# Optimization experiments

Hardware: AMD Instinct MI355X
Metric: run time of the kernel (lower is better)

Reference implementation:

```python
import jax, jax.numpy as jnp
import numpy as np

H = 4      # heads
C = 32     # out channels per head (hidden_channels)
G = 64     # num graphs


def transformer_conv(x, src, dst, Wq, bq, Wk, bk, Wv, bv, Ws, bs):
    # PyG TransformerConv, concat=False, root_weight=True, beta=False.
    N = x.shape[0]
    q = (x @ Wq + bq).reshape(N, H, C)
    k = (x @ Wk + bk).reshape(N, H, C)
    v = (x @ Wv + bv).reshape(N, H, C)
    qe = q[dst]            # [E,H,C] gather target queries
    ke = k[src]            # [E,H,C] gather source keys
    ve = v[src]            # [E,H,C] gather source values
    alpha = (qe * ke).sum(-1) / jnp.sqrt(jnp.asarray(C, x.dtype))  # [E,H]
    amax = jax.ops.segment_max(alpha, dst, num_segments=N)          # [N,H]
    a = jnp.exp(alpha - amax[dst])
    denom = jax.ops.segment_sum(a, dst, num_segments=N)             # [N,H]
    a = a / (denom[dst] + 1e-16)
    out = jax.ops.segment_sum(ve * a[..., None], dst, num_segments=N)  # [N,H,C]
    out = out.mean(axis=1)          # concat=False -> head average
    return out + x @ Ws + bs        # root skip


def setup_inputs() -> dict:
    key = jax.random.key(0)
    ks = jax.random.split(key, 24)
    N, E, Fin = 40000, 640000, 128
    x = jax.random.normal(ks[0], (N, Fin), dtype=jnp.float32)
    edge_index = jax.random.randint(ks[1], (2, E), 0, N, dtype=jnp.int64)
    batch = jnp.sort(jax.random.randint(ks[2], (N,), 0, G, dtype=jnp.int64))
    s = 0.05
    w = lambda k, shp: jax.random.normal(k, shp, dtype=jnp.float32) * s
    d = {"x": x, "edge_index": edge_index, "batch": batch,
         "Wq1": w(ks[3], (Fin, H * C)), "bq1": w(ks[4], (H * C,)),
         "Wk1": w(ks[5], (Fin, H * C)), "bk1": w(ks[6], (H * C,)),
         "Wv1": w(ks[7], (Fin, H * C)), "bv1": w(ks[8], (H * C,)),
         "Ws1": w(ks[9], (Fin, C)), "bs1": w(ks[10], (C,)),
         "Wq2": w(ks[11], (C, H * C)), "bq2": w(ks[12], (H * C,)),
         "Wk2": w(ks[13], (C, H * C)), "bk2": w(ks[14], (H * C,)),
         "Wv2": w(ks[15], (C, H * C)), "bv2": w(ks[16], (H * C,)),
         "Ws2": w(ks[17], (C, C)), "bs2": w(ks[18], (C,)),
         "Wlin": w(ks[19], (C, 16)), "blin": w(ks[20], (16,))}
    return d


def reference(x, edge_index, batch,
              Wq1, bq1, Wk1, bk1, Wv1, bv1, Ws1, bs1,
              Wq2, bq2, Wk2, bk2, Wv2, bv2, Ws2, bs2,
              Wlin, blin):
    src, dst = edge_index[0], edge_index[1]
    h = transformer_conv(x, src, dst, Wq1, bq1, Wk1, bk1, Wv1, bv1, Ws1, bs1)
    h = jax.nn.relu(h)
    h = transformer_conv(h, src, dst, Wq2, bq2, Wk2, bk2, Wv2, bv2, Ws2, bs2)
    # global mean pool over graphs
    sums = jax.ops.segment_sum(h, batch, num_segments=G)                  # [G,C]
    cnts = jax.ops.segment_sum(jnp.ones((h.shape[0],), h.dtype), batch, num_segments=G)
    pooled = sums / jnp.maximum(cnts, 1.0)[:, None]
    return pooled @ Wlin + blin
```

## Files before the change

kernel.cpp:

```cpp
#include <hip/hip_runtime.h>
#include <hip/hip_bf16.h>
#include <hip/hip_fp16.h>
#include <math.h>

#define HH 4
#define CC 32
#define HC 128
#define GG 64

typedef _Float16 f16x2 __attribute__((ext_vector_type(2)));
typedef _Float16 f16x8 __attribute__((ext_vector_type(8)));
typedef float f32x4 __attribute__((ext_vector_type(4)));

__device__ __forceinline__ f16x2 u2h(unsigned u) {
    union { unsigned u; f16x2 h; } x; x.u = u; return x.h;
}
__device__ __forceinline__ unsigned pkh(float a, float b) {
    __half2 h = __floats2half2_rn(a, b);
    union { __half2 h; unsigned u; } x; x.h = h; return x.u;
}
__device__ __forceinline__ f16x8 uq2h8(uint4 u) {
    union { uint4 u; f16x8 h; } x; x.u = u; return x.h;
}

__global__ void cvt_f2h_kernel(const float* __restrict__ in, unsigned* __restrict__ out, int n4)
{
    int i = blockIdx.x * 256 + threadIdx.x;
    if (i < n4) {
        float4 f = ((const float4*)in)[i];
        ((uint2*)out)[i] = make_uint2(pkh(f.x, f.y), pkh(f.z, f.w));
    }
}

__device__ __forceinline__ void wfrag_item(const float* __restrict__ Wq, const float* __restrict__ Wk,
    const float* __restrict__ Wv, const float* __restrict__ Ws,
    uint4* __restrict__ wfrag, int KS, int idx)
{
    int lane = idx & 63;
    int t = idx >> 6;
    int ks = t % KS, ct = t / KS;
    int r = lane & 15, g = lane >> 4;
    const float* W; int c, stride;
    if (ct < 8)       { W = Wq; c = ct * 16 + r;        stride = HC; }
    else if (ct < 16) { W = Wk; c = (ct - 8) * 16 + r;  stride = HC; }
    else if (ct < 24) { W = Wv; c = (ct - 16) * 16 + r; stride = HC; }
    else              { W = Ws; c = (ct - 24) * 16 + r; stride = CC; }
    unsigned u[4];
    #pragma unroll
    for (int jj = 0; jj < 4; ++jj) {
        int k = ks * 32 + g * 8 + jj * 2;
        u[jj] = pkh(W[(size_t)k * stride + c], W[(size_t)(k + 1) * stride + c]);
    }
    wfrag[idx] = make_uint4(u[0], u[1], u[2], u[3]);
}

__global__ void wfrag_both_kernel(
    const float* __restrict__ Wq1, const float* __restrict__ Wk1,
    const float* __restrict__ Wv1, const float* __restrict__ Ws1, uint4* __restrict__ wfrag1,
    const float* __restrict__ Wq2, const float* __restrict__ Wk2,
    const float* __restrict__ Wv2, const float* __restrict__ Ws2, uint4* __restrict__ wfrag2)
{
    int idx = blockIdx.x * 256 + threadIdx.x;
    const int N1 = 26 * 4 * 64;
    const int N2 = 26 * 1 * 64;
    if (idx < N1) wfrag_item(Wq1, Wk1, Wv1, Ws1, wfrag1, 4, idx);
    else if (idx < N1 + N2) wfrag_item(Wq2, Wk2, Wv2, Ws2, wfrag2, 1, idx - N1);
}

template<int KDIM>
__global__ __launch_bounds__(256) void qkv_mfma_kernel(
    const ushort* __restrict__ xh, const uint4* __restrict__ wfrag,
    const float* __restrict__ bq, const float* __restrict__ bk,
    const float* __restrict__ bv, const float* __restrict__ bs,
    unsigned* __restrict__ qh, uint4* __restrict__ kv4, float* __restrict__ skip,
    int N)
{
    constexpr int KS = KDIM / 32;
    const int lane = threadIdx.x & 63;
    const int wv = threadIdx.x >> 6;
    const int n0 = (blockIdx.x * 4 + wv) * 16;
    if (n0 >= N) return;
    const int r = lane & 15, g = lane >> 4;
    const int node = n0 + r;

    f16x8 a[KS];
    #pragma unroll
    for (int ks = 0; ks < KS; ++ks)
        a[ks] = uq2h8(*(const uint4*)&xh[(size_t)node * KDIM + ks * 32 + g * 8]);

    if (blockIdx.y == 0) {
        const float SC2 = 0.25500526806584186f;
        f32x4 acc[10];
        #pragma unroll
        for (int i = 0; i < 10; ++i) acc[i] = (f32x4){0.f, 0.f, 0.f, 0.f};
        #pragma unroll
        for (int i = 0; i < 8; ++i)
            #pragma unroll
            for (int ks = 0; ks < KS; ++ks) {
                f16x8 w = uq2h8(wfrag[((size_t)i * KS + ks) * 64 + lane]);
                acc[i] = __builtin_amdgcn_mfma_f32_16x16x32_f16(w, a[ks], acc[i], 0, 0, 0);
            }
        #pragma unroll
        for (int i = 0; i < 2; ++i)
            #pragma unroll
            for (int ks = 0; ks < KS; ++ks) {
                f16x8 w = uq2h8(wfrag[((size_t)(24 + i) * KS + ks) * 64 + lane]);
                acc[8 + i] = __builtin_amdgcn_mfma_f32_16x16x32_f16(w, a[ks], acc[8 + i], 0, 0, 0);
            }
        if (node < N) {
            #pragma unroll
            for (int i = 0; i < 8; ++i) {
                float4 bb = *(const float4*)&bq[i * 16 + g * 4];
                uint2 o = make_uint2(pkh((acc[i][0] + bb.x) * SC2, (acc[i][1] + bb.y) * SC2),
                                     pkh((acc[i][2] + bb.z) * SC2, (acc[i][3] + bb.w) * SC2));
                *(uint2*)&qh[(size_t)node * 64 + i * 8 + g * 2] = o;
            }
            #pragma unroll
            for (int i = 0; i < 2; ++i) {
                float4 bb = *(const float4*)&bs[i * 16 + g * 4];
                float4 o = make_float4(acc[8 + i][0] + bb.x, acc[8 + i][1] + bb.y,
                                       acc[8 + i][2] + bb.z, acc[8 + i][3] + bb.w);
                *(float4*)&skip[(size_t)node * CC + i * 16 + g * 4] = o;
            }
        }
    } else {
        f32x4 acck[8], accv[8];
        #pragma unroll
        for (int i = 0; i < 8; ++i) { acck[i] = (f32x4){0.f,0.f,0.f,0.f}; accv[i] = (f32x4){0.f,0.f,0.f,0.f}; }
        #pragma unroll
        for (int i = 0; i < 8; ++i)
            #pragma unroll
            for (int ks = 0; ks < KS; ++ks) {
                f16x8 wk = uq2h8(wfrag[((size_t)(8 + i) * KS + ks) * 64 + lane]);
                acck[i] = __builtin_amdgcn_mfma_f32_16x16x32_f16(wk, a[ks], acck[i], 0, 0, 0);
                f16x8 wvf = uq2h8(wfrag[((size_t)(16 + i) * KS + ks) * 64 + lane]);
                accv[i] = __builtin_amdgcn_mfma_f32_16x16x32_f16(wvf, a[ks], accv[i], 0, 0, 0);
            }
        if (node < N) {
            #pragma unroll
            for (int i = 0; i < 8; ++i) {
                float4 bbk = *(const float4*)&bk[i * 16 + g * 4];
                float4 bbv = *(const float4*)&bv[i * 16 + g * 4];
                uint4 o;
                o.x = pkh(acck[i][0] + bbk.x, acck[i][1] + bbk.y);
                o.y = pkh(acck[i][2] + bbk.z, acck[i][3] + bbk.w);
                o.z = pkh(accv[i][0] + bbv.x, accv[i][1] + bbv.y);
                o.w = pkh(accv[i][2] + bbv.z, accv[i][3] + bbv.w);
                kv4[(size_t)node * 32 + i * 4 + g] = o;
            }
        }
    }
}

__global__ void deg_kernel(const int* __restrict__ dst, int* __restrict__ deg, int E)
{
    int e = blockIdx.x * blockDim.x + threadIdx.x;
    if (e < E) atomicAdd(&deg[dst[e]], 1);
}

__global__ void bsum_kernel(const int* __restrict__ deg, int* __restrict__ bsum, int N)
{
    int base = blockIdx.x * 1024;
    int tid = threadIdx.x;
    int s = 0;
    for (int i = base + tid; i < base + 1024 && i < N; i += 256) s += deg[i];
    #pragma unroll
    for (int ofs = 32; ofs > 0; ofs >>= 1) s += __shfl_xor(s, ofs, 64);
    __shared__ int ws[4];
    int wid = tid >> 6;
    if ((tid & 63) == 0) ws[wid] = s;
    __syncthreads();
    if (tid == 0) bsum[blockIdx.x] = ws[0] + ws[1] + ws[2] + ws[3];
}

__global__ void bscan_kernel(int* __restrict__ bsum, int* __restrict__ off, int nb, int N)
{
    int i = threadIdx.x;
    int val = (i < nb) ? bsum[i] : 0;
    int v = val;
    #pragma unroll
    for (int ofs = 1; ofs < 64; ofs <<= 1) {
        int t = __shfl_up(v, ofs, 64);
        if (i >= ofs) v += t;
    }
    if (i < nb) bsum[i] = v - val;
    if (i == 63) off[N] = v;
}

__global__ void scan2_kernel(const int* __restrict__ deg, const int* __restrict__ bsum,
                             int* __restrict__ off, int* __restrict__ cursor, int N)
{
    int base = blockIdx.x * 1024;
    int tid = threadIdx.x;
    int idx = base + tid * 4;
    int d0 = (idx     < N) ? deg[idx]     : 0;
    int d1 = (idx + 1 < N) ? deg[idx + 1] : 0;
    int d2 = (idx + 2 < N) ? deg[idx + 2] : 0;
    int d3 = (idx + 3 < N) ? deg[idx + 3] : 0;
    int tsum = d0 + d1 + d2 + d3;
    int v = tsum;
    int lane = tid & 63;
    #pragma unroll
    for (int ofs = 1; ofs < 64; ofs <<= 1) {
        int t = __shfl_up(v, ofs, 64);
        if (lane >= ofs) v += t;
    }
    __shared__ int wsum[4];
    int wid = tid >> 6;
    if (lane == 63) wsum[wid] = v;
    __syncthreads();
    int wbase = 0;
    for (int w = 0; w < wid; ++w) wbase += wsum[w];
    int excl = bsum[blockIdx.x] + wbase + (v - tsum);
    if (idx     < N) { off[idx]     = excl;                cursor[idx]     = excl; }
    if (idx + 1 < N) { off[idx + 1] = excl + d0;           cursor[idx + 1] = excl + d0; }
    if (idx + 2 < N) { off[idx + 2] = excl + d0 + d1;      cursor[idx + 2] = excl + d0 + d1; }
    if (idx + 3 < N) { off[idx + 3] = excl + d0 + d1 + d2; cursor[idx + 3] = excl + d0 + d1 + d2; }
}

__global__ void fill_kernel(const int* __restrict__ src, const int* __restrict__ dst,
                            int* __restrict__ cursor, int* __restrict__ esrc, int E)
{
    int e = blockIdx.x * blockDim.x + threadIdx.x;
    if (e < E) {
        int d = dst[e];
        int pos = atomicAdd(&cursor[d], 1);
        esrc[pos] = src[e];
    }
}

template<int MODE>
__global__ __launch_bounds__(128) void attn_kernel(const unsigned* __restrict__ qh,
    const uint4* __restrict__ kv4, const int* __restrict__ off, const int* __restrict__ esrc,
    const float* __restrict__ skip, void* __restrict__ hout, int N)
{
    const int wave = threadIdx.x >> 6;
    const int lane = threadIdx.x & 63;
    const int n = blockIdx.x * 2 + wave;
    if (n >= N) return;
    const int half = lane >> 5;
    const int j = lane & 31;

    uint2 qv = *(const uint2*)&qh[(size_t)n * 64 + j * 2];
    f16x2 q01 = u2h(qv.x), q23 = u2h(qv.y);

    int beg = __builtin_amdgcn_readfirstlane(off[n]);
    int end = __builtin_amdgcn_readfirstlane(off[n + 1]);

    float lsum = 0.f, a0 = 0.f, a1 = 0.f, a2 = 0.f, a3 = 0.f;

    auto body = [&](int idx, bool guard) {
        int sidx = (guard && idx >= end) ? end - 1 : idx;
        int s = esrc[sidx];
        uint4 raw = kv4[(size_t)s * 32 + j];
        f16x2 k01 = u2h(raw.x), k23 = u2h(raw.y);
        f16x2 v01 = u2h(raw.z), v23 = u2h(raw.w);
#if defined(__has_builtin) && __has_builtin(__builtin_amdgcn_fdot2)
        float d = __builtin_amdgcn_fdot2(q01, k01,
                    __builtin_amdgcn_fdot2(q23, k23, 0.f, false), false);
#else
        float d = (float)q01.x*(float)k01.x + (float)q01.y*(float)k01.y
                + (float)q23.x*(float)k23.x + (float)q23.y*(float)k23.y;
#endif
        d += __shfl_xor(d, 1, 8);
        d += __shfl_xor(d, 2, 8);
        d += __shfl_xor(d, 4, 8);
        float e = exp2f(d);
        if (guard && idx >= end) e = 0.f;
        lsum += e;
        a0 = fmaf(e, (float)v01.x, a0);
        a1 = fmaf(e, (float)v01.y, a1);
        a2 = fmaf(e, (float)v23.x, a2);
        a3 = fmaf(e, (float)v23.y, a3);
    };

    int p = beg;
    for (; p + 8 <= end; p += 8) {
        body(p + half, false);
        body(p + 2 + half, false);
        body(p + 4 + half, false);
        body(p + 6 + half, false);
    }
    for (; p < end; p += 2) body(p + half, true);

    lsum += __shfl_xor(lsum, 32);
    a0 += __shfl_xor(a0, 32);
    a1 += __shfl_xor(a1, 32);
    a2 += __shfl_xor(a2, 32);
    a3 += __shfl_xor(a3, 32);

    float inv = 1.f / (lsum + 1e-16f);
    float r0 = a0 * inv, r1 = a1 * inv, r2 = a2 * inv, r3 = a3 * inv;
    r0 += __shfl_xor(r0, 8, 32);  r0 += __shfl_xor(r0, 16, 32);
    r1 += __shfl_xor(r1, 8, 32);  r1 += __shfl_xor(r1, 16, 32);
    r2 += __shfl_xor(r2, 8, 32);  r2 += __shfl_xor(r2, 16, 32);
    r3 += __shfl_xor(r3, 8, 32);  r3 += __shfl_xor(r3, 16, 32);

    if (lane < 8) {
        float4 sk = *(const float4*)&skip[(size_t)n * CC + lane * 4];
        float o0 = 0.25f * r0 + sk.x;
        float o1 = 0.25f * r1 + sk.y;
        float o2 = 0.25f * r2 + sk.z;
        float o3 = 0.25f * r3 + sk.w;
        if (MODE) {
            o0 = fmaxf(o0, 0.f); o1 = fmaxf(o1, 0.f);
            o2 = fmaxf(o2, 0.f); o3 = fmaxf(o3, 0.f);
            *(uint2*)&((unsigned*)hout)[(size_t)n * 16 + lane * 2] =
                make_uint2(pkh(o0, o1), pkh(o2, o3));
        } else {
            *(float4*)&((float*)hout)[(size_t)n * CC + lane * 4] =
                make_float4(o0, o1, o2, o3);
        }
    }
}

__global__ void pool_kernel(const float* __restrict__ h, const int* __restrict__ batch,
    float* __restrict__ sums, float* __restrict__ cntf, int N)
{
    int c = threadIdx.x & 31;
    int tn = threadIdx.x >> 5;
    int n0 = blockIdx.x * 256;
    int nend = (n0 + 256 < N) ? n0 + 256 : N;
    float acc = 0.f, cnt = 0.f;
    int curg = -1;
    for (int n = n0 + tn; n < nend; n += 8) {
        int g = batch[n];
        if (g != curg) {
            if (curg >= 0) {
                unsafeAtomicAdd(&sums[curg * CC + c], acc);
                if (c == 0) unsafeAtomicAdd(&cntf[curg], cnt);
            }
            acc = 0.f; cnt = 0.f; curg = g;
        }
        acc += h[(size_t)n * CC + c];
        cnt += 1.f;
    }
    if (curg >= 0) {
        unsafeAtomicAdd(&sums[curg * CC + c], acc);
        if (c == 0) unsafeAtomicAdd(&cntf[curg], cnt);
    }
}

__global__ void final_lin_kernel(const float* __restrict__ sums, const float* __restrict__ cntf,
    const float* __restrict__ Wlin, const float* __restrict__ blin, float* __restrict__ out)
{
    int g = blockIdx.x;
    int j = threadIdx.x;
    float cnt = fmaxf(cntf[g], 1.0f);
    float acc = 0.f;
    #pragma unroll
    for (int c = 0; c < CC; ++c)
        acc += (sums[g * CC + c] / cnt) * Wlin[c * 16 + j];
    out[g * 16 + j] = acc + blin[j];
}

extern "C" void kernel_launch(void* const* d_in, const int* in_sizes, int n_in,
                              void* d_out, int out_size, void* d_ws, size_t ws_size,
                              hipStream_t stream) {
    const float* x     = (const float*)d_in[0];
    const int*   ei    = (const int*)d_in[1];
    const int*   batch = (const int*)d_in[2];
    const float* Wq1 = (const float*)d_in[3],  *bq1 = (const float*)d_in[4];
    const float* Wk1 = (const float*)d_in[5],  *bk1 = (const float*)d_in[6];
    const float* Wv1 = (const float*)d_in[7],  *bv1 = (const float*)d_in[8];
    const float* Ws1 = (const float*)d_in[9],  *bs1 = (const float*)d_in[10];
    const float* Wq2 = (const float*)d_in[11], *bq2 = (const float*)d_in[12];
    const float* Wk2 = (const float*)d_in[13], *bk2 = (const float*)d_in[14];
    const float* Wv2 = (const float*)d_in[15], *bv2 = (const float*)d_in[16];
    const float* Ws2 = (const float*)d_in[17], *bs2 = (const float*)d_in[18];
    const float* Wlin = (const float*)d_in[19], *blin = (const float*)d_in[20];

    const int N = in_sizes[0] / 128;
    const int E = in_sizes[1] / 2;
    const int* src = ei;
    const int* dstp = ei + E;
    const int NB = (N + 1023) / 1024;
    const int Npad = (N + 63) & ~63;

    char* wp = (char*)d_ws;
    auto alloc = [&](size_t bytes) -> void* {
        void* p = wp;
        wp += (bytes + 255) & ~(size_t)255;
        return p;
    };
    unsigned* qh   = (unsigned*)alloc((size_t)N * 64 * 4);
    uint4* kv4     = (uint4*)alloc((size_t)N * 32 * 16);
    float* skip    = (float*)alloc((size_t)N * CC * 4);
    unsigned* h1h  = (unsigned*)alloc((size_t)Npad * 16 * 4);
    float* h2      = (float*)alloc((size_t)N * CC * 4);
    ushort* xh     = (ushort*)alloc((size_t)Npad * HC * 2);
    uint4* wfrag1  = (uint4*)alloc((size_t)26 * 4 * 64 * 16);
    uint4* wfrag2  = (uint4*)alloc((size_t)26 * 1 * 64 * 16);
    int* deg    = (int*)alloc((size_t)N * 4);
    int* off    = (int*)alloc((size_t)(N + 1) * 4);
    int* cursor = (int*)alloc((size_t)N * 4);
    int* esrc   = (int*)alloc((size_t)E * 4);
    int* bsum   = (int*)alloc((size_t)((NB + 63) & ~63) * 4);
    float* sums = (float*)alloc((size_t)GG * CC * 4);
    float* cntf = (float*)alloc((size_t)GG * 4);

    cvt_f2h_kernel<<<(N * HC / 4 + 255) / 256, 256, 0, stream>>>(x, (unsigned*)xh, N * HC / 4);
    wfrag_both_kernel<<<(26 * 5 * 64 + 255) / 256, 256, 0, stream>>>(
        Wq1, Wk1, Wv1, Ws1, wfrag1, Wq2, Wk2, Wv2, Ws2, wfrag2);

    hipMemsetAsync(deg, 0, (size_t)N * 4, stream);
    deg_kernel<<<(E + 255) / 256, 256, 0, stream>>>(dstp, deg, E);
    bsum_kernel<<<NB, 256, 0, stream>>>(deg, bsum, N);
    bscan_kernel<<<1, 64, 0, stream>>>(bsum, off, NB, N);
    scan2_kernel<<<NB, 256, 0, stream>>>(deg, bsum, off, cursor, N);
    fill_kernel<<<(E + 255) / 256, 256, 0, stream>>>(src, dstp, cursor, esrc, E);

    dim3 ggrid((N + 63) / 64, 2);
    dim3 agrid((N + 1) / 2);

    qkv_mfma_kernel<128><<<ggrid, 256, 0, stream>>>(xh, wfrag1, bq1, bk1, bv1, bs1,
                                                    qh, kv4, skip, N);
    attn_kernel<1><<<agrid, 128, 0, stream>>>(qh, kv4, off, esrc, skip, h1h, N);

    qkv_mfma_kernel<32><<<ggrid, 256, 0, stream>>>((const ushort*)h1h, wfrag2, bq2, bk2, bv2, bs2,
                                                   qh, kv4, skip, N);
    attn_kernel<0><<<agrid, 128, 0, stream>>>(qh, kv4, off, esrc, skip, h2, N);

    hipMemsetAsync(sums, 0, (size_t)(GG * CC + GG) * 4, stream);
    pool_kernel<<<(N + 255) / 256, 256, 0, stream>>>(h2, batch, sums, cntf, N);
    final_lin_kernel<<<GG, 16, 0, stream>>>(sums, cntf, Wlin, blin, (float*)d_out);
}
```

Baseline: 238.9 us.

## Prefetch gathered K/V rows in attention loop and fuse prep launches

The attention edge loop is now software-pipelined: the next four gathered kv rows are loaded before the current four are computed, which aims to hide gather latency. The tail loop is inlined with its guard. Separately, the fp16 conversion, weight-fragment packing, the degree zeroing and the pool-accumulator zeroing are merged into one prep kernel. This removes two memsets and one launch. The cost is higher register pressure in the attention kernel, which could lower occupancy.

```diff
diff --git a/kernel.cpp b/kernel.cpp
--- a/kernel.cpp
+++ b/kernel.cpp
@@ -21,15 +21,6 @@
 }
 __device__ __forceinline__ f16x8 uq2h8(uint4 u) {
     union { uint4 u; f16x8 h; } x; x.u = u; return x.h;
-}
-
-__global__ void cvt_f2h_kernel(const float* __restrict__ in, unsigned* __restrict__ out, int n4)
-{
-    int i = blockIdx.x * 256 + threadIdx.x;
-    if (i < n4) {
-        float4 f = ((const float4*)in)[i];
-        ((uint2*)out)[i] = make_uint2(pkh(f.x, f.y), pkh(f.z, f.w));
-    }
 }
 
 __device__ __forceinline__ void wfrag_item(const float* __restrict__ Wq, const float* __restrict__ Wk,
@@ -54,17 +45,29 @@
     wfrag[idx] = make_uint4(u[0], u[1], u[2], u[3]);
 }
 
-__global__ void wfrag_both_kernel(
+__global__ void prep_kernel(const float* __restrict__ x, unsigned* __restrict__ xh, int n4,
     const float* __restrict__ Wq1, const float* __restrict__ Wk1,
     const float* __restrict__ Wv1, const float* __restrict__ Ws1, uint4* __restrict__ wfrag1,
     const float* __restrict__ Wq2, const float* __restrict__ Wk2,
-    const float* __restrict__ Wv2, const float* __restrict__ Ws2, uint4* __restrict__ wfrag2)
-{
-    int idx = blockIdx.x * 256 + threadIdx.x;
+    const float* __restrict__ Wv2, const float* __restrict__ Ws2, uint4* __restrict__ wfrag2,
+    int* __restrict__ deg, int N, float* __restrict__ sums)
+{
     const int N1 = 26 * 4 * 64;
     const int N2 = 26 * 1 * 64;
-    if (idx < N1) wfrag_item(Wq1, Wk1, Wv1, Ws1, wfrag1, 4, idx);
-    else if (idx < N1 + N2) wfrag_item(Wq2, Wk2, Wv2, Ws2, wfrag2, 1, idx - N1);
+    int i = blockIdx.x * 256 + threadIdx.x;
+    if (i < n4) {
+        float4 f = ((const float4*)x)[i];
+        ((uint2*)xh)[i] = make_uint2(pkh(f.x, f.y), pkh(f.z, f.w));
+        return;
+    }
+    i -= n4;
+    if (i < N1) { wfrag_item(Wq1, Wk1, Wv1, Ws1, wfrag1, 4, i); return; }
+    i -= N1;
+    if (i < N2) { wfrag_item(Wq2, Wk2, Wv2, Ws2, wfrag2, 1, i); return; }
+    i -= N2;
+    if (i < N) { deg[i] = 0; return; }
+    i -= N;
+    if (i < GG * CC + GG) sums[i] = 0.f;
 }
 
 template<int KDIM>
@@ -249,10 +252,7 @@
 
     float lsum = 0.f, a0 = 0.f, a1 = 0.f, a2 = 0.f, a3 = 0.f;
 
-    auto body = [&](int idx, bool guard) {
-        int sidx = (guard && idx >= end) ? end - 1 : idx;
-        int s = esrc[sidx];
-        uint4 raw = kv4[(size_t)s * 32 + j];
+    auto compute = [&](uint4 raw) {
         f16x2 k01 = u2h(raw.x), k23 = u2h(raw.y);
         f16x2 v01 = u2h(raw.z), v23 = u2h(raw.w);
 #if defined(__has_builtin) && __has_builtin(__builtin_amdgcn_fdot2)
@@ -266,22 +266,51 @@
         d += __shfl_xor(d, 2, 8);
         d += __shfl_xor(d, 4, 8);
         float e = exp2f(d);
-        if (guard && idx >= end) e = 0.f;
         lsum += e;
         a0 = fmaf(e, (float)v01.x, a0);
         a1 = fmaf(e, (float)v01.y, a1);
         a2 = fmaf(e, (float)v23.x, a2);
         a3 = fmaf(e, (float)v23.y, a3);
     };
+    auto ld = [&](int p2) -> uint4 {
+        return kv4[(size_t)esrc[p2 + half] * 32 + j];
+    };
 
     int p = beg;
-    for (; p + 8 <= end; p += 8) {
-        body(p + half, false);
-        body(p + 2 + half, false);
-        body(p + 4 + half, false);
-        body(p + 6 + half, false);
-    }
-    for (; p < end; p += 2) body(p + half, true);
+    if (p + 8 <= end) {
+        uint4 c0 = ld(p), c1 = ld(p + 2), c2 = ld(p + 4), c3 = ld(p + 6);
+        p += 8;
+        for (; p + 8 <= end; p += 8) {
+            uint4 n0 = ld(p), n1 = ld(p + 2), n2 = ld(p + 4), n3 = ld(p + 6);
+            compute(c0); compute(c1); compute(c2); compute(c3);
+            c0 = n0; c1 = n1; c2 = n2; c3 = n3;
+        }
+        compute(c0); compute(c1); compute(c2); compute(c3);
+    }
+    for (; p < end; p += 2) {
+        int idx = p + half;
+        int sidx = (idx >= end) ? end - 1 : idx;
+        uint4 raw = kv4[(size_t)esrc[sidx] * 32 + j];
+        f16x2 k01 = u2h(raw.x), k23 = u2h(raw.y);
+        f16x2 v01 = u2h(raw.z), v23 = u2h(raw.w);
+#if defined(__has_builtin) && __has_builtin(__builtin_amdgcn_fdot2)
+        float d = __builtin_amdgcn_fdot2(q01, k01,
+                    __builtin_amdgcn_fdot2(q23, k23, 0.f, false), false);
+#else
+        float d = (float)q01.x*(float)k01.x + (float)q01.y*(float)k01.y
+                + (float)q23.x*(float)k23.x + (float)q23.y*(float)k23.y;
+#endif
+        d += __shfl_xor(d, 1, 8);
+        d += __shfl_xor(d, 2, 8);
+        d += __shfl_xor(d, 4, 8);
+        float e = exp2f(d);
+        if (idx >= end) e = 0.f;
+        lsum += e;
+        a0 = fmaf(e, (float)v01.x, a0);
+        a1 = fmaf(e, (float)v01.y, a1);
+        a2 = fmaf(e, (float)v23.x, a2);
+        a3 = fmaf(e, (float)v23.y, a3);
+    }
 
     lsum += __shfl_xor(lsum, 32);
     a0 += __shfl_xor(a0, 32);
@@ -399,11 +428,13 @@
     float* sums = (float*)alloc((size_t)GG * CC * 4);
     float* cntf = (float*)alloc((size_t)GG * 4);
 
-    cvt_f2h_kernel<<<(N * HC / 4 + 255) / 256, 256, 0, stream>>>(x, (unsigned*)xh, N * HC / 4);
-    wfrag_both_kernel<<<(26 * 5 * 64 + 255) / 256, 256, 0, stream>>>(
-        Wq1, Wk1, Wv1, Ws1, wfrag1, Wq2, Wk2, Wv2, Ws2, wfrag2);
-
-    hipMemsetAsync(deg, 0, (size_t)N * 4, stream);
+    const int n4 = N * HC / 4;
+    const int prep_total = n4 + 26 * 5 * 64 + N + GG * CC + GG;
+    prep_kernel<<<(prep_total + 255) / 256, 256, 0, stream>>>(
+        x, (unsigned*)xh, n4,
+        Wq1, Wk1, Wv1, Ws1, wfrag1, Wq2, Wk2, Wv2, Ws2, wfrag2,
+        deg, N, sums);
+
     deg_kernel<<<(E + 255) / 256, 256, 0, stream>>>(dstp, deg, E);
     bsum_kernel<<<NB, 256, 0, stream>>>(deg, bsum, N);
     bscan_kernel<<<1, 64, 0, stream>>>(bsum, off, NB, N);
@@ -421,7 +452,6 @@
                                                    qh, kv4, skip, N);
     attn_kernel<0><<<agrid, 128, 0, stream>>>(qh, kv4, off, esrc, skip, h2, N);
 
-    hipMemsetAsync(sums, 0, (size_t)(GG * CC + GG) * 4, stream);
     pool_kernel<<<(N + 255) / 256, 256, 0, stream>>>(h2, batch, sums, cntf, N);
     final_lin_kernel<<<GG, 16, 0, stream>>>(sums, cntf, Wlin, blin, (float*)d_out);
 }
```

Measured after the change: 232.1 us (median of 2 runs). 1.03x faster.
